# Kernel tuning notes

Hardware: AMD Instinct MI355X
Metric: run time of the kernel (lower is better)

Reference implementation:

```python
import jax, jax.numpy as jnp
import numpy as np

N, F_DIM, H, MAX_STEPS = 768, 256, 128, 100


def normalize_adj(adj):
    # add self loops, symmetric normalization D^{-1/2} (A+I) D^{-1/2}
    a = adj + jnp.eye(adj.shape[0], dtype=adj.dtype)
    d = a.sum(axis=-1)
    d_inv_sqrt = jnp.where(d > 0, jax.lax.rsqrt(d), 0.0)
    return d_inv_sqrt[:, None] * a * d_inv_sqrt[None, :]


def gcn_layer(h, a_norm, weight):
    return jax.nn.relu(a_norm @ h @ weight)


def setup_inputs() -> dict:
    key = jax.random.key(0)
    ks = jax.random.split(key, 8)
    xavier = lambda k, shp: jax.random.uniform(k, shp, jnp.float32,
                                               -np.sqrt(6.0 / (shp[0] + shp[1])),
                                               np.sqrt(6.0 / (shp[0] + shp[1])))
    return {
        "x": jax.random.normal(ks[0], (N, F_DIM), jnp.float32),
        "adj_noisy": jax.random.uniform(ks[1], (N, N), jnp.float32),
        "w1": xavier(ks[2], (F_DIM, H)),
        "w2": xavier(ks[3], (H, H)),
        "time_emb": jax.random.normal(ks[4], (MAX_STEPS, H), jnp.float32),
        "we1": xavier(ks[5], (3 * H, H)),
        "be1": jnp.zeros((H,), jnp.float32),
        "we2": xavier(ks[6], (H, 1)),
        "be2": jnp.zeros((1,), jnp.float32),
        "t": 50,
    }


def reference(x, adj_noisy, w1, w2, time_emb, we1, be1, we2, be2, t):
    a_norm = normalize_adj(adj_noisy)
    h = gcn_layer(x, a_norm, w1)            # (N, H)
    h = gcn_layer(h, a_norm, w2)            # (N, H)
    t_emb = time_emb[t]                     # (H,)
    # edge_mlp layer 1 on concat([h_i, h_j, t_emb]) decomposed to avoid (N,N,3H):
    # concat @ we1 == h_i @ we1[:H] + h_j @ we1[H:2H] + t_emb @ we1[2H:]
    p = h @ we1[:H]                         # (N, H) contribution from h_i
    q = h @ we1[H:2 * H]                    # (N, H) contribution from h_j
    c = t_emb @ we1[2 * H:] + be1           # (H,)  contribution from t_emb + bias
    z = jax.nn.relu(p[:, None, :] + q[None, :, :] + c)   # (N, N, H)
    logits = (z @ we2)[..., 0] + be2[0]     # (N, N)
    adj_pred = jax.nn.sigmoid(logits)
    return (adj_pred + adj_pred.T) / 2
```

## Files before the change

### kernel.cpp

```cpp
#include <hip/hip_runtime.h>

#define NN 768
#define FD 256
#define HD 128

__device__ __forceinline__ float relu(float x) { return x > 0.f ? x : 0.f; }
__device__ __forceinline__ void fma4(float4& a, float s, float4 v) {
    a.x = fmaf(s, v.x, a.x); a.y = fmaf(s, v.y, a.y);
    a.z = fmaf(s, v.z, a.z); a.w = fmaf(s, v.w, a.w);
}
__device__ __forceinline__ float rdot(float4 a, float4 b, float4 w) {
    float s = relu(a.x + b.x) * w.x;
    s = fmaf(relu(a.y + b.y), w.y, s);
    s = fmaf(relu(a.z + b.z), w.z, s);
    s = fmaf(relu(a.w + b.w), w.w, s);
    return s;
}

__global__ __launch_bounds__(768) void k_prep(
        const float* __restrict__ x, const float* __restrict__ adj,
        const float* __restrict__ w1, const float* __restrict__ temb,
        const float* __restrict__ we1, const float* __restrict__ be1,
        const int* __restrict__ tptr, float* __restrict__ dinv,
        float* __restrict__ cvec, float* __restrict__ t1D) {
    int b = blockIdx.x, tid = threadIdx.x;
    if (b == 256) {
        __shared__ float ts[HD];
        if (tid < HD) ts[tid] = temb[tptr[0] * HD + tid];
        __syncthreads();
        if (tid < HD) {
            float a0 = be1[tid], a1 = 0.f, a2 = 0.f, a3 = 0.f;
            for (int m = 0; m < HD; m += 4) {
                a0 = fmaf(ts[m + 0], we1[(2 * HD + m + 0) * HD + tid], a0);
                a1 = fmaf(ts[m + 1], we1[(2 * HD + m + 1) * HD + tid], a1);
                a2 = fmaf(ts[m + 2], we1[(2 * HD + m + 2) * HD + tid], a2);
                a3 = fmaf(ts[m + 3], we1[(2 * HD + m + 3) * HD + tid], a3);
            }
            cvec[tid] = (a0 + a1) + (a2 + a3);
        }
        return;
    }
    int i0 = b * 3;
    __shared__ float xs[3][FD];
    __shared__ float part[3][2][HD];
    __shared__ float red[12];
    __shared__ float sdi[3];
    if (tid < 192) {
        int row = tid >> 6, m4 = tid & 63;
        *(float4*)&xs[row][m4 * 4] = *(const float4*)&x[(i0 + row) * FD + m4 * 4];
    }
    {
        int r2 = tid >> 8, s = tid & 255;
        float sum = 0.f;
        if (s < 192) {
            float4 a = *(const float4*)&adj[(i0 + r2) * NN + s * 4];
            sum = (a.x + a.y) + (a.z + a.w);
        }
#pragma unroll
        for (int off = 32; off > 0; off >>= 1) sum += __shfl_down(sum, off, 64);
        if ((tid & 63) == 0) red[tid >> 6] = sum;
    }
    __syncthreads();
    if (tid < 3) {
        float t = (red[4 * tid] + red[4 * tid + 1]) + (red[4 * tid + 2] + red[4 * tid + 3]);
        float d = rsqrtf(t + 1.f);
        sdi[tid] = d; dinv[i0 + tid] = d;
    }
    __syncthreads();
    int r = tid >> 8, half = (tid >> 7) & 1, k = tid & 127;
    float a0 = 0.f, a1 = 0.f, a2 = 0.f, a3 = 0.f;
    for (int g = 128 * half; g < 128 * half + 128; g += 16) {
        float wv[16];
#pragma unroll
        for (int u = 0; u < 16; ++u) wv[u] = w1[(g + u) * HD + k];
#pragma unroll
        for (int u = 0; u < 16; ++u) {
            float xv = xs[r][g + u];
            if ((u & 3) == 0) a0 = fmaf(xv, wv[u], a0);
            else if ((u & 3) == 1) a1 = fmaf(xv, wv[u], a1);
            else if ((u & 3) == 2) a2 = fmaf(xv, wv[u], a2);
            else a3 = fmaf(xv, wv[u], a3);
        }
    }
    part[r][half][k] = (a0 + a1) + (a2 + a3);
    __syncthreads();
    if (half == 0) t1D[(i0 + r) * HD + k] = sdi[r] * (part[r][0][k] + part[r][1][k]);
}

__global__ __launch_bounds__(256) void k_agg(const float* __restrict__ adj,
                                             const float* __restrict__ tin,
                                             float* __restrict__ P) {
    int it = blockIdx.x % 24, seg = blockIdx.x / 24;
    int i0 = it * 32, j0 = seg * 48;
    __shared__ float adjS[32][52];
    __shared__ float TS[48][132];
    int tid = threadIdx.x;
    for (int f = tid; f < 384; f += 256) {
        int r = f / 12, c4 = f % 12;
        *(float4*)&adjS[r][c4 * 4] = *(const float4*)&adj[(i0 + r) * NN + j0 + c4 * 4];
    }
    for (int f = tid; f < 1536; f += 256) {
        int r = f >> 5, c4 = f & 31;
        *(float4*)&TS[r][c4 * 4] = *(const float4*)&tin[(j0 + r) * HD + c4 * 4];
    }
    __syncthreads();
    int tk = tid & 31, tr = tid >> 5;
    float4 acc0 = {0,0,0,0}, acc1 = {0,0,0,0}, acc2 = {0,0,0,0}, acc3 = {0,0,0,0};
#pragma unroll 6
    for (int j = 0; j < 48; ++j) {
        float4 tv = *(float4*)&TS[j][tk * 4];
        fma4(acc0, adjS[tr * 4 + 0][j], tv);
        fma4(acc1, adjS[tr * 4 + 1][j], tv);
        fma4(acc2, adjS[tr * 4 + 2][j], tv);
        fma4(acc3, adjS[tr * 4 + 3][j], tv);
    }
    float* base = P + (size_t)seg * (NN * HD) + (i0 + tr * 4) * HD + tk * 4;
    *(float4*)&base[0 * HD] = acc0;
    *(float4*)&base[1 * HD] = acc1;
    *(float4*)&base[2 * HD] = acc2;
    *(float4*)&base[3 * HD] = acc3;
}

__global__ __launch_bounds__(384) void k_fin_w(
        const float* __restrict__ P, const float* __restrict__ tin,
        const float* __restrict__ dinv, const float* __restrict__ w2,
        float* __restrict__ outD) {
    __shared__ float gs[3][HD];
    __shared__ float part[3][4][HD];
    int tid = threadIdx.x, i0 = blockIdx.x * 3;
    {
        int r = tid >> 7, k = tid & 127;
        int i = i0 + r;
        float s = tin[i * HD + k];
#pragma unroll
        for (int seg = 0; seg < 16; ++seg) s += P[(size_t)seg * (NN * HD) + i * HD + k];
        gs[r][k] = relu(dinv[i] * s);
    }
    __syncthreads();
    int r = tid >> 7, ms = (tid >> 5) & 3, kq = tid & 31;
    const float4* w24 = (const float4*)w2;
    float4 acc = {0,0,0,0};
#pragma unroll
    for (int u = 0; u < 32; ++u) {
        int m = ms * 32 + u;
        fma4(acc, gs[r][m], w24[m * 32 + kq]);
    }
    *(float4*)&part[r][ms][kq * 4] = acc;
    __syncthreads();
    int k = tid & 127;
    float s = part[r][0][k] + part[r][1][k] + part[r][2][k] + part[r][3][k];
    outD[(i0 + r) * HD + k] = dinv[i0 + r] * s;
}

__global__ __launch_bounds__(384) void k_fin_pq(
        const float* __restrict__ P, const float* __restrict__ tin,
        const float* __restrict__ dinv, const float* __restrict__ we1,
        const float* __restrict__ cvec, float* __restrict__ p, float* __restrict__ q) {
    __shared__ float gs[3][HD];
    __shared__ float part[3][8][HD];
    int tid = threadIdx.x, i0 = blockIdx.x * 3;
    {
        int r = tid >> 7, k = tid & 127;
        int i = i0 + r;
        float s = tin[i * HD + k];
#pragma unroll
        for (int seg = 0; seg < 16; ++seg) s += P[(size_t)seg * (NN * HD) + i * HD + k];
        gs[r][k] = relu(dinv[i] * s);
    }
    __syncthreads();
    int r = tid >> 7, ms = (tid >> 5) & 3, kq = tid & 31;
    const float4* we14 = (const float4*)we1;
    float4 ap = {0,0,0,0}, aq = {0,0,0,0};
#pragma unroll
    for (int u = 0; u < 32; ++u) {
        int m = ms * 32 + u;
        float g = gs[r][m];
        fma4(ap, g, we14[m * 32 + kq]);
        fma4(aq, g, we14[(HD + m) * 32 + kq]);
    }
    *(float4*)&part[r][ms][kq * 4] = ap;
    *(float4*)&part[r][ms + 4][kq * 4] = aq;
    __syncthreads();
    int k = tid & 127;
    float sp = part[r][0][k] + part[r][1][k] + part[r][2][k] + part[r][3][k];
    float sq = part[r][4][k] + part[r][5][k] + part[r][6][k] + part[r][7][k];
    p[(i0 + r) * HD + k] = cvec[k] + sp;
    q[(i0 + r) * HD + k] = sq;
}

__global__ __launch_bounds__(256) void k_pair(
        const float* __restrict__ p, const float* __restrict__ q,
        const float* __restrict__ we2, const float* __restrict__ be2,
        float* __restrict__ out) {
    int t = blockIdx.x;
    int bj = (int)((sqrtf(8.f * t + 1.f) - 1.f) * 0.5f);
    while ((bj + 1) * (bj + 2) / 2 <= t) ++bj;
    while (bj * (bj + 1) / 2 > t) --bj;
    int bi = t - bj * (bj + 1) / 2;
    int i0 = bi * 32, j0 = bj * 32;
    __shared__ float spi[32][68], sqi[32][68], spj[32][68], sqj[32][68];
    __shared__ float w2s[HD];
    int tid = threadIdx.x;
    int tx = tid & 15, ty = tid >> 4;
    if (tid < HD) w2s[tid] = we2[tid];
    float accij[2][2] = {{0.f, 0.f}, {0.f, 0.f}};
    float accji[2][2] = {{0.f, 0.f}, {0.f, 0.f}};
    for (int h = 0; h < 2; ++h) {
        __syncthreads();
        int kb = h * 64;
        for (int idx = tid; idx < 512; idx += 256) {
            int r = idx >> 4, c4 = idx & 15;
            *(float4*)&spi[r][c4 * 4] = *(const float4*)&p[(i0 + r) * HD + kb + c4 * 4];
            *(float4*)&sqi[r][c4 * 4] = *(const float4*)&q[(i0 + r) * HD + kb + c4 * 4];
            *(float4*)&spj[r][c4 * 4] = *(const float4*)&p[(j0 + r) * HD + kb + c4 * 4];
            *(float4*)&sqj[r][c4 * 4] = *(const float4*)&q[(j0 + r) * HD + kb + c4 * 4];
        }
        __syncthreads();
#pragma unroll 8
        for (int k4 = 0; k4 < 16; ++k4) {
            float4 w = *(float4*)&w2s[kb + k4 * 4];
            float4 Pi0 = *(float4*)&spi[2 * ty + 0][k4 * 4];
            float4 Pi1 = *(float4*)&spi[2 * ty + 1][k4 * 4];
            float4 Qi0 = *(float4*)&sqi[2 * ty + 0][k4 * 4];
            float4 Qi1 = *(float4*)&sqi[2 * ty + 1][k4 * 4];
            float4 Pj0 = *(float4*)&spj[2 * tx + 0][k4 * 4];
            float4 Pj1 = *(float4*)&spj[2 * tx + 1][k4 * 4];
            float4 Qj0 = *(float4*)&sqj[2 * tx + 0][k4 * 4];
            float4 Qj1 = *(float4*)&sqj[2 * tx + 1][k4 * 4];
            accij[0][0] += rdot(Pi0, Qj0, w); accji[0][0] += rdot(Pj0, Qi0, w);
            accij[0][1] += rdot(Pi0, Qj1, w); accji[0][1] += rdot(Pj1, Qi0, w);
            accij[1][0] += rdot(Pi1, Qj0, w); accji[1][0] += rdot(Pj0, Qi1, w);
            accij[1][1] += rdot(Pi1, Qj1, w); accji[1][1] += rdot(Pj1, Qi1, w);
        }
    }
    float bias = be2[0];
#pragma unroll
    for (int e = 0; e < 2; ++e)
#pragma unroll
        for (int f = 0; f < 2; ++f) {
            int i = i0 + 2 * ty + e, j = j0 + 2 * tx + f;
            float lij = accij[e][f] + bias, lji = accji[e][f] + bias;
            float v = 0.5f * (1.f / (1.f + __expf(-lij)) + 1.f / (1.f + __expf(-lji)));
            out[i * NN + j] = v;
            out[j * NN + i] = v;
        }
}

extern "C" void kernel_launch(void* const* d_in, const int* in_sizes, int n_in,
                              void* d_out, int out_size, void* d_ws, size_t ws_size,
                              hipStream_t stream) {
    const float* x    = (const float*)d_in[0];
    const float* adj  = (const float*)d_in[1];
    const float* w1   = (const float*)d_in[2];
    const float* w2   = (const float*)d_in[3];
    const float* temb = (const float*)d_in[4];
    const float* we1  = (const float*)d_in[5];
    const float* be1  = (const float*)d_in[6];
    const float* we2  = (const float*)d_in[7];
    const float* be2  = (const float*)d_in[8];
    const int* tptr   = (const int*)d_in[9];
    float* out        = (float*)d_out;

    float* ws   = (float*)d_ws;
    float* dinv = ws;
    float* c    = ws + 768;
    float* A    = ws + 1024;
    float* B    = A + NN * HD;
    float* C    = B + NN * HD;
    float* P    = C + NN * HD;

    k_prep  <<<257, 768, 0, stream>>>(x, adj, w1, temb, we1, be1, tptr, dinv, c, A);
    k_agg   <<<384, 256, 0, stream>>>(adj, A, P);
    k_fin_w <<<256, 384, 0, stream>>>(P, A, dinv, w2, B);
    k_agg   <<<384, 256, 0, stream>>>(adj, B, P);
    k_fin_pq<<<256, 384, 0, stream>>>(P, B, dinv, we1, c, A, C);
    k_pair  <<<300, 256, 0, stream>>>(A, C, we2, be2, out);
}
```

Measured before the change: 126.8 us.

## Fuse all GCN and edge-MLP stages into one persistent kernel with grid barriers

Replaces the six separate kernel launches with a single 300-block persistent kernel that moves between phases through atomic-counter grid barriers. The counters are zeroed with a memset. Aggregation is restructured so each block computes full adjacency rows times the feature matrix directly, which removes the 16-way partial-sum buffer and its reduction pass. The goal is to cut launch gaps and global round-trips. The cost is lower parallelism in the aggregation phases (256 blocks each doing full-length dot products) and reliance on all 300 blocks being co-resident for the spin barriers.

Result: slower. 407.6 us (+221.5%).

```diff
diff --git a/kernel.cpp b/kernel.cpp
--- a/kernel.cpp
+++ b/kernel.cpp
@@ -3,6 +3,7 @@
 #define NN 768
 #define FD 256
 #define HD 128
+#define NBLK 300
 
 __device__ __forceinline__ float relu(float x) { return x > 0.f ? x : 0.f; }
 __device__ __forceinline__ void fma4(float4& a, float s, float4 v) {
@@ -17,233 +18,218 @@
     return s;
 }
 
-__global__ __launch_bounds__(768) void k_prep(
+struct S1mem { float xs[3][FD]; float ts[HD]; float sdi[4]; };
+struct S2mem { float adjT[NN][4]; float part[8][3][HD]; float gs[3][HD]; };
+struct S4mem { float pi[32][68]; float qi[32][68]; float pj[32][68]; float qj[32][68]; float w2s[HD]; };
+union SMem { S1mem s1; S2mem s2; S4mem s4; };
+
+__device__ __forceinline__ void gsync(int* cnt) {
+    __threadfence();
+    __syncthreads();
+    if (threadIdx.x == 0) {
+        atomicAdd(cnt, 1);
+        while (__hip_atomic_load(cnt, __ATOMIC_ACQUIRE, __HIP_MEMORY_SCOPE_AGENT) < NBLK)
+            __builtin_amdgcn_s_sleep(2);
+    }
+    __syncthreads();
+    __threadfence();
+}
+
+__device__ __forceinline__ void gcn_gs(SMem& sm, const float* __restrict__ adj,
+                                       const float* __restrict__ tin,
+                                       const float* __restrict__ dinv, int i0, int tid) {
+    for (int idx = tid; idx < 3 * NN; idx += 256) {
+        int r = idx / NN, j = idx - r * NN;
+        sm.s2.adjT[j][r] = adj[(i0 + r) * NN + j];
+    }
+    __syncthreads();
+    int k4 = tid & 31, jc = tid >> 5;
+    float4 a0 = {0,0,0,0}, a1 = {0,0,0,0}, a2 = {0,0,0,0};
+    const float* tbase = tin + k4 * 4;
+#pragma unroll 4
+    for (int jj = 0; jj < 96; ++jj) {
+        int j = jc * 96 + jj;
+        float4 av = *(float4*)&sm.s2.adjT[j][0];
+        float4 tv = *(const float4*)&tbase[j * HD];
+        fma4(a0, av.x, tv);
+        fma4(a1, av.y, tv);
+        fma4(a2, av.z, tv);
+    }
+    *(float4*)&sm.s2.part[jc][0][k4 * 4] = a0;
+    *(float4*)&sm.s2.part[jc][1][k4 * 4] = a1;
+    *(float4*)&sm.s2.part[jc][2][k4 * 4] = a2;
+    __syncthreads();
+    for (int idx = tid; idx < 3 * HD; idx += 256) {
+        int r = idx >> 7, k = idx & 127;
+        float s = tin[(i0 + r) * HD + k];
+#pragma unroll
+        for (int c = 0; c < 8; ++c) s += sm.s2.part[c][r][k];
+        sm.s2.gs[r][k] = relu(dinv[i0 + r] * s);
+    }
+    __syncthreads();
+}
+
+__global__ __launch_bounds__(256, 2) void fused(
         const float* __restrict__ x, const float* __restrict__ adj,
-        const float* __restrict__ w1, const float* __restrict__ temb,
-        const float* __restrict__ we1, const float* __restrict__ be1,
-        const int* __restrict__ tptr, float* __restrict__ dinv,
-        float* __restrict__ cvec, float* __restrict__ t1D) {
+        const float* __restrict__ w1, const float* __restrict__ w2,
+        const float* __restrict__ temb, const float* __restrict__ we1,
+        const float* __restrict__ be1, const float* __restrict__ we2,
+        const float* __restrict__ be2, const int* __restrict__ tptr,
+        float* __restrict__ ws, float* __restrict__ out) {
+    __shared__ SMem sm;
     int b = blockIdx.x, tid = threadIdx.x;
-    if (b == 256) {
-        __shared__ float ts[HD];
-        if (tid < HD) ts[tid] = temb[tptr[0] * HD + tid];
+    int* cnt = (int*)ws;
+    float* dinv = ws + 16;
+    float* cvec = ws + 800;
+    float* t1 = ws + 1024;
+    float* t2 = t1 + NN * HD;
+    float* p  = t2 + NN * HD;
+    float* q  = p + NN * HD;
+
+    if (b < 256) {
+        int i0 = 3 * b;
+        for (int idx = tid; idx < 192; idx += 256) {
+            int r = idx >> 6, c4 = idx & 63;
+            *(float4*)&sm.s1.xs[r][c4 * 4] = *(const float4*)&x[(i0 + r) * FD + c4 * 4];
+        }
+        int wv = tid >> 6, ln = tid & 63;
+        if (wv < 3) {
+            const float4* ar = (const float4*)&adj[(i0 + wv) * NN];
+            float4 A0 = ar[ln], A1 = ar[ln + 64], A2 = ar[ln + 128];
+            float s = ((A0.x + A0.y) + (A0.z + A0.w)) + ((A1.x + A1.y) + (A1.z + A1.w))
+                    + ((A2.x + A2.y) + (A2.z + A2.w));
+#pragma unroll
+            for (int off = 32; off > 0; off >>= 1) s += __shfl_down(s, off, 64);
+            if (ln == 0) sm.s1.sdi[wv] = rsqrtf(s + 1.f);
+        }
+        __syncthreads();
+        if (tid < 3) dinv[i0 + tid] = sm.s1.sdi[tid];
+        int k = tid & 127, mh = tid >> 7;
+        float ac0 = 0.f, ac1 = 0.f, ac2 = 0.f;
+        const float* wcol = w1 + k;
+#pragma unroll 4
+        for (int m = mh * 128; m < mh * 128 + 128; ++m) {
+            float wval = wcol[m * HD];
+            ac0 = fmaf(sm.s1.xs[0][m], wval, ac0);
+            ac1 = fmaf(sm.s1.xs[1][m], wval, ac1);
+            ac2 = fmaf(sm.s1.xs[2][m], wval, ac2);
+        }
+        __syncthreads();
+        float* tmp = &sm.s1.xs[0][0];
+        tmp[mh * 384 + 0 * 128 + k] = ac0;
+        tmp[mh * 384 + 1 * 128 + k] = ac1;
+        tmp[mh * 384 + 2 * 128 + k] = ac2;
+        __syncthreads();
+        for (int idx = tid; idx < 384; idx += 256) {
+            int r = idx >> 7, kk = idx & 127;
+            t1[(i0 + r) * HD + kk] = sm.s1.sdi[r] * (tmp[r * 128 + kk] + tmp[384 + r * 128 + kk]);
+        }
+    } else if (b == 256) {
+        if (tid < HD) sm.s1.ts[tid] = temb[tptr[0] * HD + tid];
         __syncthreads();
         if (tid < HD) {
-            float a0 = be1[tid], a1 = 0.f, a2 = 0.f, a3 = 0.f;
-            for (int m = 0; m < HD; m += 4) {
-                a0 = fmaf(ts[m + 0], we1[(2 * HD + m + 0) * HD + tid], a0);
-                a1 = fmaf(ts[m + 1], we1[(2 * HD + m + 1) * HD + tid], a1);
-                a2 = fmaf(ts[m + 2], we1[(2 * HD + m + 2) * HD + tid], a2);
-                a3 = fmaf(ts[m + 3], we1[(2 * HD + m + 3) * HD + tid], a3);
-            }
-            cvec[tid] = (a0 + a1) + (a2 + a3);
-        }
-        return;
-    }
-    int i0 = b * 3;
-    __shared__ float xs[3][FD];
-    __shared__ float part[3][2][HD];
-    __shared__ float red[12];
-    __shared__ float sdi[3];
-    if (tid < 192) {
-        int row = tid >> 6, m4 = tid & 63;
-        *(float4*)&xs[row][m4 * 4] = *(const float4*)&x[(i0 + row) * FD + m4 * 4];
-    }
+            float a = be1[tid];
+#pragma unroll 4
+            for (int m = 0; m < HD; ++m)
+                a = fmaf(sm.s1.ts[m], we1[(2 * HD + m) * HD + tid], a);
+            cvec[tid] = a;
+        }
+    }
+    gsync(&cnt[0]);
+
+    if (b < 256) {
+        int i0 = 3 * b;
+        gcn_gs(sm, adj, t1, dinv, i0, tid);
+        for (int idx = tid; idx < 3 * HD; idx += 256) {
+            int r = idx >> 7, k = idx & 127;
+            float acc = 0.f;
+            const float* wc = w2 + k;
+#pragma unroll
+            for (int m4 = 0; m4 < 32; ++m4) {
+                float4 gv = *(float4*)&sm.s2.gs[r][m4 * 4];
+                acc = fmaf(gv.x, wc[(m4 * 4 + 0) * HD], acc);
+                acc = fmaf(gv.y, wc[(m4 * 4 + 1) * HD], acc);
+                acc = fmaf(gv.z, wc[(m4 * 4 + 2) * HD], acc);
+                acc = fmaf(gv.w, wc[(m4 * 4 + 3) * HD], acc);
+            }
+            t2[(i0 + r) * HD + k] = dinv[i0 + r] * acc;
+        }
+    }
+    gsync(&cnt[1]);
+
+    if (b < 256) {
+        int i0 = 3 * b;
+        gcn_gs(sm, adj, t2, dinv, i0, tid);
+        for (int idx = tid; idx < 3 * HD; idx += 256) {
+            int r = idx >> 7, k = idx & 127;
+            float ap = 0.f, aq = 0.f;
+            const float* wp = we1 + k;
+            const float* wq = we1 + HD * HD + k;
+#pragma unroll
+            for (int m4 = 0; m4 < 32; ++m4) {
+                float4 gv = *(float4*)&sm.s2.gs[r][m4 * 4];
+                ap = fmaf(gv.x, wp[(m4 * 4 + 0) * HD], ap); aq = fmaf(gv.x, wq[(m4 * 4 + 0) * HD], aq);
+                ap = fmaf(gv.y, wp[(m4 * 4 + 1) * HD], ap); aq = fmaf(gv.y, wq[(m4 * 4 + 1) * HD], aq);
+                ap = fmaf(gv.z, wp[(m4 * 4 + 2) * HD], ap); aq = fmaf(gv.z, wq[(m4 * 4 + 2) * HD], aq);
+                ap = fmaf(gv.w, wp[(m4 * 4 + 3) * HD], ap); aq = fmaf(gv.w, wq[(m4 * 4 + 3) * HD], aq);
+            }
+            p[(i0 + r) * HD + k] = ap + cvec[k];
+            q[(i0 + r) * HD + k] = aq;
+        }
+    }
+    gsync(&cnt[2]);
+
     {
-        int r2 = tid >> 8, s = tid & 255;
-        float sum = 0.f;
-        if (s < 192) {
-            float4 a = *(const float4*)&adj[(i0 + r2) * NN + s * 4];
-            sum = (a.x + a.y) + (a.z + a.w);
-        }
-#pragma unroll
-        for (int off = 32; off > 0; off >>= 1) sum += __shfl_down(sum, off, 64);
-        if ((tid & 63) == 0) red[tid >> 6] = sum;
-    }
-    __syncthreads();
-    if (tid < 3) {
-        float t = (red[4 * tid] + red[4 * tid + 1]) + (red[4 * tid + 2] + red[4 * tid + 3]);
-        float d = rsqrtf(t + 1.f);
-        sdi[tid] = d; dinv[i0 + tid] = d;
-    }
-    __syncthreads();
-    int r = tid >> 8, half = (tid >> 7) & 1, k = tid & 127;
-    float a0 = 0.f, a1 = 0.f, a2 = 0.f, a3 = 0.f;
-    for (int g = 128 * half; g < 128 * half + 128; g += 16) {
-        float wv[16];
-#pragma unroll
-        for (int u = 0; u < 16; ++u) wv[u] = w1[(g + u) * HD + k];
-#pragma unroll
-        for (int u = 0; u < 16; ++u) {
-            float xv = xs[r][g + u];
-            if ((u & 3) == 0) a0 = fmaf(xv, wv[u], a0);
-            else if ((u & 3) == 1) a1 = fmaf(xv, wv[u], a1);
-            else if ((u & 3) == 2) a2 = fmaf(xv, wv[u], a2);
-            else a3 = fmaf(xv, wv[u], a3);
-        }
-    }
-    part[r][half][k] = (a0 + a1) + (a2 + a3);
-    __syncthreads();
-    if (half == 0) t1D[(i0 + r) * HD + k] = sdi[r] * (part[r][0][k] + part[r][1][k]);
-}
-
-__global__ __launch_bounds__(256) void k_agg(const float* __restrict__ adj,
-                                             const float* __restrict__ tin,
-                                             float* __restrict__ P) {
-    int it = blockIdx.x % 24, seg = blockIdx.x / 24;
-    int i0 = it * 32, j0 = seg * 48;
-    __shared__ float adjS[32][52];
-    __shared__ float TS[48][132];
-    int tid = threadIdx.x;
-    for (int f = tid; f < 384; f += 256) {
-        int r = f / 12, c4 = f % 12;
-        *(float4*)&adjS[r][c4 * 4] = *(const float4*)&adj[(i0 + r) * NN + j0 + c4 * 4];
-    }
-    for (int f = tid; f < 1536; f += 256) {
-        int r = f >> 5, c4 = f & 31;
-        *(float4*)&TS[r][c4 * 4] = *(const float4*)&tin[(j0 + r) * HD + c4 * 4];
-    }
-    __syncthreads();
-    int tk = tid & 31, tr = tid >> 5;
-    float4 acc0 = {0,0,0,0}, acc1 = {0,0,0,0}, acc2 = {0,0,0,0}, acc3 = {0,0,0,0};
-#pragma unroll 6
-    for (int j = 0; j < 48; ++j) {
-        float4 tv = *(float4*)&TS[j][tk * 4];
-        fma4(acc0, adjS[tr * 4 + 0][j], tv);
-        fma4(acc1, adjS[tr * 4 + 1][j], tv);
-        fma4(acc2, adjS[tr * 4 + 2][j], tv);
-        fma4(acc3, adjS[tr * 4 + 3][j], tv);
-    }
-    float* base = P + (size_t)seg * (NN * HD) + (i0 + tr * 4) * HD + tk * 4;
-    *(float4*)&base[0 * HD] = acc0;
-    *(float4*)&base[1 * HD] = acc1;
-    *(float4*)&base[2 * HD] = acc2;
-    *(float4*)&base[3 * HD] = acc3;
-}
-
-__global__ __launch_bounds__(384) void k_fin_w(
-        const float* __restrict__ P, const float* __restrict__ tin,
-        const float* __restrict__ dinv, const float* __restrict__ w2,
-        float* __restrict__ outD) {
-    __shared__ float gs[3][HD];
-    __shared__ float part[3][4][HD];
-    int tid = threadIdx.x, i0 = blockIdx.x * 3;
-    {
-        int r = tid >> 7, k = tid & 127;
-        int i = i0 + r;
-        float s = tin[i * HD + k];
-#pragma unroll
-        for (int seg = 0; seg < 16; ++seg) s += P[(size_t)seg * (NN * HD) + i * HD + k];
-        gs[r][k] = relu(dinv[i] * s);
-    }
-    __syncthreads();
-    int r = tid >> 7, ms = (tid >> 5) & 3, kq = tid & 31;
-    const float4* w24 = (const float4*)w2;
-    float4 acc = {0,0,0,0};
-#pragma unroll
-    for (int u = 0; u < 32; ++u) {
-        int m = ms * 32 + u;
-        fma4(acc, gs[r][m], w24[m * 32 + kq]);
-    }
-    *(float4*)&part[r][ms][kq * 4] = acc;
-    __syncthreads();
-    int k = tid & 127;
-    float s = part[r][0][k] + part[r][1][k] + part[r][2][k] + part[r][3][k];
-    outD[(i0 + r) * HD + k] = dinv[i0 + r] * s;
-}
-
-__global__ __launch_bounds__(384) void k_fin_pq(
-        const float* __restrict__ P, const float* __restrict__ tin,
-        const float* __restrict__ dinv, const float* __restrict__ we1,
-        const float* __restrict__ cvec, float* __restrict__ p, float* __restrict__ q) {
-    __shared__ float gs[3][HD];
-    __shared__ float part[3][8][HD];
-    int tid = threadIdx.x, i0 = blockIdx.x * 3;
-    {
-        int r = tid >> 7, k = tid & 127;
-        int i = i0 + r;
-        float s = tin[i * HD + k];
-#pragma unroll
-        for (int seg = 0; seg < 16; ++seg) s += P[(size_t)seg * (NN * HD) + i * HD + k];
-        gs[r][k] = relu(dinv[i] * s);
-    }
-    __syncthreads();
-    int r = tid >> 7, ms = (tid >> 5) & 3, kq = tid & 31;
-    const float4* we14 = (const float4*)we1;
-    float4 ap = {0,0,0,0}, aq = {0,0,0,0};
-#pragma unroll
-    for (int u = 0; u < 32; ++u) {
-        int m = ms * 32 + u;
-        float g = gs[r][m];
-        fma4(ap, g, we14[m * 32 + kq]);
-        fma4(aq, g, we14[(HD + m) * 32 + kq]);
-    }
-    *(float4*)&part[r][ms][kq * 4] = ap;
-    *(float4*)&part[r][ms + 4][kq * 4] = aq;
-    __syncthreads();
-    int k = tid & 127;
-    float sp = part[r][0][k] + part[r][1][k] + part[r][2][k] + part[r][3][k];
-    float sq = part[r][4][k] + part[r][5][k] + part[r][6][k] + part[r][7][k];
-    p[(i0 + r) * HD + k] = cvec[k] + sp;
-    q[(i0 + r) * HD + k] = sq;
-}
-
-__global__ __launch_bounds__(256) void k_pair(
-        const float* __restrict__ p, const float* __restrict__ q,
-        const float* __restrict__ we2, const float* __restrict__ be2,
-        float* __restrict__ out) {
-    int t = blockIdx.x;
-    int bj = (int)((sqrtf(8.f * t + 1.f) - 1.f) * 0.5f);
-    while ((bj + 1) * (bj + 2) / 2 <= t) ++bj;
-    while (bj * (bj + 1) / 2 > t) --bj;
-    int bi = t - bj * (bj + 1) / 2;
-    int i0 = bi * 32, j0 = bj * 32;
-    __shared__ float spi[32][68], sqi[32][68], spj[32][68], sqj[32][68];
-    __shared__ float w2s[HD];
-    int tid = threadIdx.x;
-    int tx = tid & 15, ty = tid >> 4;
-    if (tid < HD) w2s[tid] = we2[tid];
-    float accij[2][2] = {{0.f, 0.f}, {0.f, 0.f}};
-    float accji[2][2] = {{0.f, 0.f}, {0.f, 0.f}};
-    for (int h = 0; h < 2; ++h) {
-        __syncthreads();
-        int kb = h * 64;
-        for (int idx = tid; idx < 512; idx += 256) {
-            int r = idx >> 4, c4 = idx & 15;
-            *(float4*)&spi[r][c4 * 4] = *(const float4*)&p[(i0 + r) * HD + kb + c4 * 4];
-            *(float4*)&sqi[r][c4 * 4] = *(const float4*)&q[(i0 + r) * HD + kb + c4 * 4];
-            *(float4*)&spj[r][c4 * 4] = *(const float4*)&p[(j0 + r) * HD + kb + c4 * 4];
-            *(float4*)&sqj[r][c4 * 4] = *(const float4*)&q[(j0 + r) * HD + kb + c4 * 4];
-        }
-        __syncthreads();
+        int t = b;
+        int bj = (int)((sqrtf(8.f * t + 1.f) - 1.f) * 0.5f);
+        while ((bj + 1) * (bj + 2) / 2 <= t) ++bj;
+        while (bj * (bj + 1) / 2 > t) --bj;
+        int bi = t - bj * (bj + 1) / 2;
+        int i0 = bi * 32, j0 = bj * 32;
+        int tx = tid & 15, ty = tid >> 4;
+        if (tid < HD) sm.s4.w2s[tid] = we2[tid];
+        float accij[2][2] = {{0.f, 0.f}, {0.f, 0.f}};
+        float accji[2][2] = {{0.f, 0.f}, {0.f, 0.f}};
+        for (int h = 0; h < 2; ++h) {
+            __syncthreads();
+            int kb = h * 64;
+            for (int idx = tid; idx < 512; idx += 256) {
+                int r = idx >> 4, c4 = idx & 15;
+                *(float4*)&sm.s4.pi[r][c4 * 4] = *(const float4*)&p[(i0 + r) * HD + kb + c4 * 4];
+                *(float4*)&sm.s4.qi[r][c4 * 4] = *(const float4*)&q[(i0 + r) * HD + kb + c4 * 4];
+                *(float4*)&sm.s4.pj[r][c4 * 4] = *(const float4*)&p[(j0 + r) * HD + kb + c4 * 4];
+                *(float4*)&sm.s4.qj[r][c4 * 4] = *(const float4*)&q[(j0 + r) * HD + kb + c4 * 4];
+            }
+            __syncthreads();
 #pragma unroll 8
-        for (int k4 = 0; k4 < 16; ++k4) {
-            float4 w = *(float4*)&w2s[kb + k4 * 4];
-            float4 Pi0 = *(float4*)&spi[2 * ty + 0][k4 * 4];
-            float4 Pi1 = *(float4*)&spi[2 * ty + 1][k4 * 4];
-            float4 Qi0 = *(float4*)&sqi[2 * ty + 0][k4 * 4];
-            float4 Qi1 = *(float4*)&sqi[2 * ty + 1][k4 * 4];
-            float4 Pj0 = *(float4*)&spj[2 * tx + 0][k4 * 4];
-            float4 Pj1 = *(float4*)&spj[2 * tx + 1][k4 * 4];
-            float4 Qj0 = *(float4*)&sqj[2 * tx + 0][k4 * 4];
-            float4 Qj1 = *(float4*)&sqj[2 * tx + 1][k4 * 4];
-            accij[0][0] += rdot(Pi0, Qj0, w); accji[0][0] += rdot(Pj0, Qi0, w);
-            accij[0][1] += rdot(Pi0, Qj1, w); accji[0][1] += rdot(Pj1, Qi0, w);
-            accij[1][0] += rdot(Pi1, Qj0, w); accji[1][0] += rdot(Pj0, Qi1, w);
-            accij[1][1] += rdot(Pi1, Qj1, w); accji[1][1] += rdot(Pj1, Qi1, w);
-        }
-    }
-    float bias = be2[0];
-#pragma unroll
-    for (int e = 0; e < 2; ++e)
-#pragma unroll
-        for (int f = 0; f < 2; ++f) {
-            int i = i0 + 2 * ty + e, j = j0 + 2 * tx + f;
-            float lij = accij[e][f] + bias, lji = accji[e][f] + bias;
-            float v = 0.5f * (1.f / (1.f + __expf(-lij)) + 1.f / (1.f + __expf(-lji)));
-            out[i * NN + j] = v;
-            out[j * NN + i] = v;
-        }
+            for (int k4 = 0; k4 < 16; ++k4) {
+                float4 w = *(float4*)&sm.s4.w2s[kb + k4 * 4];
+                float4 Pi0 = *(float4*)&sm.s4.pi[2 * ty + 0][k4 * 4];
+                float4 Pi1 = *(float4*)&sm.s4.pi[2 * ty + 1][k4 * 4];
+                float4 Qi0 = *(float4*)&sm.s4.qi[2 * ty + 0][k4 * 4];
+                float4 Qi1 = *(float4*)&sm.s4.qi[2 * ty + 1][k4 * 4];
+                float4 Pj0 = *(float4*)&sm.s4.pj[2 * tx + 0][k4 * 4];
+                float4 Pj1 = *(float4*)&sm.s4.pj[2 * tx + 1][k4 * 4];
+                float4 Qj0 = *(float4*)&sm.s4.qj[2 * tx + 0][k4 * 4];
+                float4 Qj1 = *(float4*)&sm.s4.qj[2 * tx + 1][k4 * 4];
+                accij[0][0] += rdot(Pi0, Qj0, w); accji[0][0] += rdot(Pj0, Qi0, w);
+                accij[0][1] += rdot(Pi0, Qj1, w); accji[0][1] += rdot(Pj1, Qi0, w);
+                accij[1][0] += rdot(Pi1, Qj0, w); accji[1][0] += rdot(Pj0, Qi1, w);
+                accij[1][1] += rdot(Pi1, Qj1, w); accji[1][1] += rdot(Pj1, Qi1, w);
+            }
+        }
+        float bias = be2[0];
+#pragma unroll
+        for (int e = 0; e < 2; ++e)
+#pragma unroll
+            for (int f = 0; f < 2; ++f) {
+                int i = i0 + 2 * ty + e, j = j0 + 2 * tx + f;
+                float lij = accij[e][f] + bias, lji = accji[e][f] + bias;
+                float v = 0.5f * (1.f / (1.f + __expf(-lij)) + 1.f / (1.f + __expf(-lji)));
+                out[i * NN + j] = v;
+                out[j * NN + i] = v;
+            }
+    }
 }
 
 extern "C" void kernel_launch(void* const* d_in, const int* in_sizes, int n_in,
@@ -260,19 +246,8 @@
     const float* be2  = (const float*)d_in[8];
     const int* tptr   = (const int*)d_in[9];
     float* out        = (float*)d_out;
-
-    float* ws   = (float*)d_ws;
-    float* dinv = ws;
-    float* c    = ws + 768;
-    float* A    = ws + 1024;
-    float* B    = A + NN * HD;
-    float* C    = B + NN * HD;
-    float* P    = C + NN * HD;
-
-    k_prep  <<<257, 768, 0, stream>>>(x, adj, w1, temb, we1, be1, tptr, dinv, c, A);
-    k_agg   <<<384, 256, 0, stream>>>(adj, A, P);
-    k_fin_w <<<256, 384, 0, stream>>>(P, A, dinv, w2, B);
-    k_agg   <<<384, 256, 0, stream>>>(adj, B, P);
-    k_fin_pq<<<256, 384, 0, stream>>>(P, B, dinv, we1, c, A, C);
-    k_pair  <<<300, 256, 0, stream>>>(A, C, we2, be2, out);
-}
+    float* ws         = (float*)d_ws;
+
+    hipMemsetAsync(d_ws, 0, 16, stream);
+    fused<<<NBLK, 256, 0, stream>>>(x, adj, w1, w2, temb, we1, be1, we2, be2, tptr, ws, out);
+}
```

## Fuse GCN aggregation with weight projection, removing split-K partial buffer

Applied to the files above, without the earlier changes.

Replaces the split-K aggregation kernel plus separate finalize kernels with two fused layer kernels. Each block handles three rows, stages their adjacency rows in shared memory, reduces over all 768 neighbours across eight warps, and applies the dense weight projection in the same kernel. This removes two launches and the 16-slice partial-sum buffer round trip through global memory. In exchange each block streams the whole 768x128 feature matrix from global/L2 with no shared-memory tiling, and the weight matvec is now scalar.

After: 126.4 us. Within noise of the previous version (-0.3%).

```diff
diff --git a/kernel.cpp b/kernel.cpp
--- a/kernel.cpp
+++ b/kernel.cpp
@@ -87,105 +87,92 @@
     if (half == 0) t1D[(i0 + r) * HD + k] = sdi[r] * (part[r][0][k] + part[r][1][k]);
 }
 
-__global__ __launch_bounds__(256) void k_agg(const float* __restrict__ adj,
-                                             const float* __restrict__ tin,
-                                             float* __restrict__ P) {
-    int it = blockIdx.x % 24, seg = blockIdx.x / 24;
-    int i0 = it * 32, j0 = seg * 48;
-    __shared__ float adjS[32][52];
-    __shared__ float TS[48][132];
-    int tid = threadIdx.x;
-    for (int f = tid; f < 384; f += 256) {
-        int r = f / 12, c4 = f % 12;
-        *(float4*)&adjS[r][c4 * 4] = *(const float4*)&adj[(i0 + r) * NN + j0 + c4 * 4];
-    }
-    for (int f = tid; f < 1536; f += 256) {
-        int r = f >> 5, c4 = f & 31;
-        *(float4*)&TS[r][c4 * 4] = *(const float4*)&tin[(j0 + r) * HD + c4 * 4];
-    }
-    __syncthreads();
-    int tk = tid & 31, tr = tid >> 5;
-    float4 acc0 = {0,0,0,0}, acc1 = {0,0,0,0}, acc2 = {0,0,0,0}, acc3 = {0,0,0,0};
-#pragma unroll 6
-    for (int j = 0; j < 48; ++j) {
-        float4 tv = *(float4*)&TS[j][tk * 4];
-        fma4(acc0, adjS[tr * 4 + 0][j], tv);
-        fma4(acc1, adjS[tr * 4 + 1][j], tv);
-        fma4(acc2, adjS[tr * 4 + 2][j], tv);
-        fma4(acc3, adjS[tr * 4 + 3][j], tv);
-    }
-    float* base = P + (size_t)seg * (NN * HD) + (i0 + tr * 4) * HD + tk * 4;
-    *(float4*)&base[0 * HD] = acc0;
-    *(float4*)&base[1 * HD] = acc1;
-    *(float4*)&base[2 * HD] = acc2;
-    *(float4*)&base[3 * HD] = acc3;
-}
-
-__global__ __launch_bounds__(384) void k_fin_w(
-        const float* __restrict__ P, const float* __restrict__ tin,
+__device__ __forceinline__ void gcn_agg(
+        float* __restrict__ a0s, float* __restrict__ a1s, float* __restrict__ a2s,
+        float (*part)[3][HD], float (*gs)[HD],
+        const float* __restrict__ adj, const float* __restrict__ tin,
+        const float* __restrict__ dinv, int i0, int tid) {
+    for (int j = tid; j < NN; j += 256) {
+        a0s[j] = adj[(i0 + 0) * NN + j];
+        a1s[j] = adj[(i0 + 1) * NN + j];
+        a2s[j] = adj[(i0 + 2) * NN + j];
+    }
+    __syncthreads();
+    int k4 = tid & 31, jc = tid >> 5;
+    float4 acc0 = {0,0,0,0}, acc1 = {0,0,0,0}, acc2 = {0,0,0,0};
+    const float* tb = tin + k4 * 4;
+#pragma unroll 4
+    for (int jj = 0; jj < 96; ++jj) {
+        int j = jc * 96 + jj;
+        float4 tv = *(const float4*)&tb[j * HD];
+        fma4(acc0, a0s[j], tv);
+        fma4(acc1, a1s[j], tv);
+        fma4(acc2, a2s[j], tv);
+    }
+    *(float4*)&part[jc][0][k4 * 4] = acc0;
+    *(float4*)&part[jc][1][k4 * 4] = acc1;
+    *(float4*)&part[jc][2][k4 * 4] = acc2;
+    __syncthreads();
+    for (int idx = tid; idx < 3 * HD; idx += 256) {
+        int r = idx >> 7, k = idx & 127;
+        float s = tin[(i0 + r) * HD + k];
+#pragma unroll
+        for (int c = 0; c < 8; ++c) s += part[c][r][k];
+        gs[r][k] = relu(dinv[i0 + r] * s);
+    }
+    __syncthreads();
+}
+
+__global__ __launch_bounds__(256) void k_layer1(
+        const float* __restrict__ adj, const float* __restrict__ t1,
         const float* __restrict__ dinv, const float* __restrict__ w2,
-        float* __restrict__ outD) {
+        float* __restrict__ t2) {
+    __shared__ float a0s[NN], a1s[NN], a2s[NN];
+    __shared__ float part[8][3][HD];
     __shared__ float gs[3][HD];
-    __shared__ float part[3][4][HD];
     int tid = threadIdx.x, i0 = blockIdx.x * 3;
-    {
-        int r = tid >> 7, k = tid & 127;
-        int i = i0 + r;
-        float s = tin[i * HD + k];
-#pragma unroll
-        for (int seg = 0; seg < 16; ++seg) s += P[(size_t)seg * (NN * HD) + i * HD + k];
-        gs[r][k] = relu(dinv[i] * s);
-    }
-    __syncthreads();
-    int r = tid >> 7, ms = (tid >> 5) & 3, kq = tid & 31;
-    const float4* w24 = (const float4*)w2;
-    float4 acc = {0,0,0,0};
-#pragma unroll
-    for (int u = 0; u < 32; ++u) {
-        int m = ms * 32 + u;
-        fma4(acc, gs[r][m], w24[m * 32 + kq]);
-    }
-    *(float4*)&part[r][ms][kq * 4] = acc;
-    __syncthreads();
-    int k = tid & 127;
-    float s = part[r][0][k] + part[r][1][k] + part[r][2][k] + part[r][3][k];
-    outD[(i0 + r) * HD + k] = dinv[i0 + r] * s;
-}
-
-__global__ __launch_bounds__(384) void k_fin_pq(
-        const float* __restrict__ P, const float* __restrict__ tin,
+    gcn_agg(a0s, a1s, a2s, part, gs, adj, t1, dinv, i0, tid);
+    for (int idx = tid; idx < 3 * HD; idx += 256) {
+        int r = idx >> 7, k = idx & 127;
+        float acc = 0.f;
+        const float* wc = w2 + k;
+#pragma unroll
+        for (int m4 = 0; m4 < 32; ++m4) {
+            float4 gv = *(float4*)&gs[r][m4 * 4];
+            acc = fmaf(gv.x, wc[(m4 * 4 + 0) * HD], acc);
+            acc = fmaf(gv.y, wc[(m4 * 4 + 1) * HD], acc);
+            acc = fmaf(gv.z, wc[(m4 * 4 + 2) * HD], acc);
+            acc = fmaf(gv.w, wc[(m4 * 4 + 3) * HD], acc);
+        }
+        t2[(i0 + r) * HD + k] = dinv[i0 + r] * acc;
+    }
+}
+
+__global__ __launch_bounds__(256) void k_layer2(
+        const float* __restrict__ adj, const float* __restrict__ t2,
         const float* __restrict__ dinv, const float* __restrict__ we1,
         const float* __restrict__ cvec, float* __restrict__ p, float* __restrict__ q) {
+    __shared__ float a0s[NN], a1s[NN], a2s[NN];
+    __shared__ float part[8][3][HD];
     __shared__ float gs[3][HD];
-    __shared__ float part[3][8][HD];
     int tid = threadIdx.x, i0 = blockIdx.x * 3;
-    {
-        int r = tid >> 7, k = tid & 127;
-        int i = i0 + r;
-        float s = tin[i * HD + k];
-#pragma unroll
-        for (int seg = 0; seg < 16; ++seg) s += P[(size_t)seg * (NN * HD) + i * HD + k];
-        gs[r][k] = relu(dinv[i] * s);
-    }
-    __syncthreads();
-    int r = tid >> 7, ms = (tid >> 5) & 3, kq = tid & 31;
-    const float4* we14 = (const float4*)we1;
-    float4 ap = {0,0,0,0}, aq = {0,0,0,0};
-#pragma unroll
-    for (int u = 0; u < 32; ++u) {
-        int m = ms * 32 + u;
-        float g = gs[r][m];
-        fma4(ap, g, we14[m * 32 + kq]);
-        fma4(aq, g, we14[(HD + m) * 32 + kq]);
-    }
-    *(float4*)&part[r][ms][kq * 4] = ap;
-    *(float4*)&part[r][ms + 4][kq * 4] = aq;
-    __syncthreads();
-    int k = tid & 127;
-    float sp = part[r][0][k] + part[r][1][k] + part[r][2][k] + part[r][3][k];
-    float sq = part[r][4][k] + part[r][5][k] + part[r][6][k] + part[r][7][k];
-    p[(i0 + r) * HD + k] = cvec[k] + sp;
-    q[(i0 + r) * HD + k] = sq;
+    gcn_agg(a0s, a1s, a2s, part, gs, adj, t2, dinv, i0, tid);
+    for (int idx = tid; idx < 3 * HD; idx += 256) {
+        int r = idx >> 7, k = idx & 127;
+        float ap = 0.f, aq = 0.f;
+        const float* wp = we1 + k;
+        const float* wq = we1 + HD * HD + k;
+#pragma unroll
+        for (int m4 = 0; m4 < 32; ++m4) {
+            float4 gv = *(float4*)&gs[r][m4 * 4];
+            ap = fmaf(gv.x, wp[(m4 * 4 + 0) * HD], ap); aq = fmaf(gv.x, wq[(m4 * 4 + 0) * HD], aq);
+            ap = fmaf(gv.y, wp[(m4 * 4 + 1) * HD], ap); aq = fmaf(gv.y, wq[(m4 * 4 + 1) * HD], aq);
+            ap = fmaf(gv.z, wp[(m4 * 4 + 2) * HD], ap); aq = fmaf(gv.z, wq[(m4 * 4 + 2) * HD], aq);
+            ap = fmaf(gv.w, wp[(m4 * 4 + 3) * HD], ap); aq = fmaf(gv.w, wq[(m4 * 4 + 3) * HD], aq);
+        }
+        p[(i0 + r) * HD + k] = ap + cvec[k];
+        q[(i0 + r) * HD + k] = aq;
+    }
 }
 
 __global__ __launch_bounds__(256) void k_pair(
@@ -263,16 +250,14 @@
 
     float* ws   = (float*)d_ws;
     float* dinv = ws;
-    float* c    = ws + 768;
-    float* A    = ws + 1024;
-    float* B    = A + NN * HD;
-    float* C    = B + NN * HD;
-    float* P    = C + NN * HD;
-
-    k_prep  <<<257, 768, 0, stream>>>(x, adj, w1, temb, we1, be1, tptr, dinv, c, A);
-    k_agg   <<<384, 256, 0, stream>>>(adj, A, P);
-    k_fin_w <<<256, 384, 0, stream>>>(P, A, dinv, w2, B);
-    k_agg   <<<384, 256, 0, stream>>>(adj, B, P);
-    k_fin_pq<<<256, 384, 0, stream>>>(P, B, dinv, we1, c, A, C);
-    k_pair  <<<300, 256, 0, stream>>>(A, C, we2, be2, out);
-}
+    float* cvec = ws + 768;
+    float* t1   = ws + 1024;
+    float* t2   = t1 + NN * HD;
+    float* p    = t2 + NN * HD;
+    float* q    = p + NN * HD;
+
+    k_prep  <<<257, 768, 0, stream>>>(x, adj, w1, temb, we1, be1, tptr, dinv, cvec, t1);
+    k_layer1<<<256, 256, 0, stream>>>(adj, t1, dinv, w2, t2);
+    k_layer2<<<256, 256, 0, stream>>>(adj, t2, dinv, we1, cvec, p, q);
+    k_pair  <<<300, 256, 0, stream>>>(p, q, we2, be2, out);
+}
```
